# Kernel optimization log

Hardware: AMD Instinct MI355X
Metric: run time of the kernel (lower is better)

Reference implementation:

```python
import jax, jax.numpy as jnp
import numpy as np
from jax import lax

H = W = 96
C = 3
N_PIX = H * W
N_PER_CLASS = 50   # min(size_sample_fg=100 -> shuffled to min_samples, size_sample_bg=50)
K = 5
THRESHOLD = 0.3
POS_WEIGHT = 100.0
CLEAN_THRESH = 0.6


def _sample_idx(key, valid_mask_flat, n):
    # Uniform random sample of n indices from valid positions (fixed-shape
    # replacement for tf.random.shuffle(tf.where(mask))[:n]).
    u = jax.random.uniform(key, (N_PIX,))
    score = jnp.where(valid_mask_flat, u, -1.0)
    _, idx = lax.top_k(score, n)
    return idx


def _pixel_features(img01):
    # img01: [H, W, C] in [0, 1]. Matches: reshape(img)/255 concat weighted positions.
    img_flat = img01.reshape(-1, C) / 255.0
    ii, jj = jnp.meshgrid(jnp.arange(H), jnp.arange(W), indexing='ij')
    pos = jnp.stack([ii, jj], axis=-1).reshape(-1, 2).astype(jnp.float32)
    pos = pos / jnp.array([H, W], jnp.float32) * POS_WEIGHT
    return jnp.concatenate([img_flat, pos], axis=1)  # [N_PIX, C+2]


def _process_image(img, key):
    # preprocess: (already 96x96x3) normalize & clip
    img_p = jnp.clip(img / 255.0, 0.0, 1.0)

    # extract_image_tf: clean image, pick fg/bg scribble pixels
    img_norm = img_p / jnp.max(img_p, axis=(0, 1), keepdims=True)
    cleaned = img_norm * (img_norm < CLEAN_THRESH).astype(jnp.float32)
    fg = jnp.any(cleaned > 0, axis=-1).reshape(-1)  # [N_PIX] bool
    bg = ~fg
    k_fg, k_bg = jax.random.split(key)
    fg_idx = _sample_idx(k_fg, fg, N_PER_CLASS)
    bg_idx = _sample_idx(k_bg, bg, N_PER_CLASS)

    # extract_features_tf
    feats_all = _pixel_features(img_p)                       # [N_PIX, 5]
    train_feats = jnp.concatenate([feats_all[fg_idx], feats_all[bg_idx]], axis=0)  # [100, 5]
    train_labels = jnp.concatenate([jnp.ones(N_PER_CLASS), jnp.zeros(N_PER_CLASS)])

    # segment_image_KNN_tf: standardize, brute-force cdist, top-k, label vote
    mean = jnp.mean(train_feats, axis=0)
    std = jnp.std(train_feats, axis=0)
    train_s = (train_feats - mean) / std                     # [100, 5]
    test_s = (feats_all - mean) / std                        # [N_PIX, 5]
    dist = jnp.sqrt(jnp.sum(jnp.square(test_s[:, None, :] - train_s[None, :, :]), axis=2))  # [N_PIX, 100]
    _, knn_idx = lax.top_k(-dist, K)                         # smallest-k distances
    probas = jnp.mean(train_labels[knn_idx], axis=1)         # [N_PIX]
    seg = (probas >= THRESHOLD).astype(jnp.int32).reshape(H, W)

    # mask original (preprocessed) image
    return jnp.where(seg[..., None] == 1, img_p, jnp.zeros_like(img_p))


def setup_inputs() -> dict:
    key = jax.random.key(0)
    images = jax.random.uniform(key, (32, H, W, C), dtype=jnp.float32)
    return {"images": images}


def reference(images):
    B = images.shape[0]
    keys = jax.random.split(jax.random.key(42), B)
    return jax.vmap(_process_image)(images, keys)
```

## Files before the change

### kernel.cpp

```cpp
#include <hip/hip_runtime.h>
#include <stdint.h>

#define NPIX 9216
#define NIMG 32

__device__ __forceinline__ uint32_t rotl32(uint32_t x, int d){ return (x<<d)|(x>>(32-d)); }

__device__ __forceinline__ void threefry(uint32_t k0, uint32_t k1, uint32_t x0, uint32_t x1,
                                         uint32_t &o0, uint32_t &o1){
  uint32_t ks2 = k0 ^ k1 ^ 0x1BD11BDAu;
  x0 += k0; x1 += k1;
  x0+=x1; x1=rotl32(x1,13); x1^=x0;
  x0+=x1; x1=rotl32(x1,15); x1^=x0;
  x0+=x1; x1=rotl32(x1,26); x1^=x0;
  x0+=x1; x1=rotl32(x1,6);  x1^=x0;
  x0+=k1; x1+=ks2+1u;
  x0+=x1; x1=rotl32(x1,17); x1^=x0;
  x0+=x1; x1=rotl32(x1,29); x1^=x0;
  x0+=x1; x1=rotl32(x1,16); x1^=x0;
  x0+=x1; x1=rotl32(x1,24); x1^=x0;
  x0+=ks2; x1+=k0+2u;
  x0+=x1; x1=rotl32(x1,13); x1^=x0;
  x0+=x1; x1=rotl32(x1,15); x1^=x0;
  x0+=x1; x1=rotl32(x1,26); x1^=x0;
  x0+=x1; x1=rotl32(x1,6);  x1^=x0;
  x0+=k0; x1+=k1+3u;
  x0+=x1; x1=rotl32(x1,17); x1^=x0;
  x0+=x1; x1=rotl32(x1,29); x1^=x0;
  x0+=x1; x1=rotl32(x1,16); x1^=x0;
  x0+=x1; x1=rotl32(x1,24); x1^=x0;
  x0+=k1; x1+=ks2+4u;
  x0+=x1; x1=rotl32(x1,13); x1^=x0;
  x0+=x1; x1=rotl32(x1,15); x1^=x0;
  x0+=x1; x1=rotl32(x1,26); x1^=x0;
  x0+=x1; x1=rotl32(x1,6);  x1^=x0;
  x0+=ks2; x1+=k0+5u;
  o0=x0; o1=x1;
}

__device__ __forceinline__ float clip01_div255(float x){
  return fminf(fmaxf(x/255.0f, 0.0f), 1.0f);
}

__global__ __launch_bounds__(1024) void kprep(const float* __restrict__ in,
                                              float* __restrict__ ts2g,
                                              float* __restrict__ meanstd){
#pragma clang fp contract(off)
  int img = blockIdx.x;
  int tid = threadIdx.x;

  __shared__ uint32_t vvL[NPIX];
  __shared__ uint64_t cand[2048];
  __shared__ int      hist[2][129];
  __shared__ int      nc, bbinL[2];
  __shared__ float    cmaxL[3];
  __shared__ float    wred[3][16];
  __shared__ int      tIdx[100];
  __shared__ float    feat[100][5];
  __shared__ float    mv[5], sv[5];

  if(tid<258) ((int*)hist)[tid]=0;

  const float* p = in + (size_t)img*NPIX*3;

  {
    float m0=0.f, m1=0.f, m2=0.f;
    for(int k=0;k<9;k++){
      int px = k*1024 + tid;
      m0 = fmaxf(m0, clip01_div255(p[px*3+0]));
      m1 = fmaxf(m1, clip01_div255(p[px*3+1]));
      m2 = fmaxf(m2, clip01_div255(p[px*3+2]));
    }
    for(int off=32; off>0; off>>=1){
      m0 = fmaxf(m0, __shfl_down(m0,off));
      m1 = fmaxf(m1, __shfl_down(m1,off));
      m2 = fmaxf(m2, __shfl_down(m2,off));
    }
    int lane = tid & 63, wv = tid >> 6;
    if(lane==0){ wred[0][wv]=m0; wred[1][wv]=m1; wred[2][wv]=m2; }
  }
  __syncthreads();
  if(tid<3){
    float m = wred[tid][0];
    for(int w=1;w<16;w++) m = fmaxf(m, wred[tid][w]);
    cmaxL[tid]=m;
  }
  __syncthreads();
  float c0=cmaxL[0], c1=cmaxL[1], c2=cmaxL[2];

  uint32_t ik0, ik1; threefry(0u, 42u, 0u, (uint32_t)img, ik0, ik1);
  uint32_t sf0, sf1; threefry(ik0, ik1, 0u, 0u, sf0, sf1);
  uint32_t sb0, sb1; threefry(ik0, ik1, 0u, 1u, sb0, sb1);

  for(int k=0;k<9;k++){
    int px = k*1024 + tid;
    float a  = clip01_div255(p[px*3+0])/c0;
    float bb = clip01_div255(p[px*3+1])/c1;
    float c  = clip01_div255(p[px*3+2])/c2;
    bool fg = (a>0.f && a<0.6f) || (bb>0.f && bb<0.6f) || (c>0.f && c<0.6f);
    uint32_t k0 = fg ? sf0 : sb0, k1 = fg ? sf1 : sb1;
    uint32_t r1, r2; threefry(k0, k1, 0u, (uint32_t)px, r1, r2);
    uint32_t vv = ((r1 ^ r2) >> 9) + 1u;
    vvL[px] = vv | (fg ? 0x80000000u : 0u);
    atomicAdd(&hist[fg?0:1][vv>>16], 1);
  }
  __syncthreads();

  if(tid<128){
    int cls = tid>>6, l = tid&63;
    int h0 = hist[cls][2*l];
    int h1 = hist[cls][2*l+1];
    int h128 = hist[cls][128];
    int S = h0 + h1;
    for(int off=1; off<64; off<<=1){
      int o = __shfl_down(S, off);
      if(l + off < 64) S += o;
    }
    int ss0 = S + h128;
    int ss1 = S - h0 + h128;
    int cd = -1;
    if(ss0 >= 50) cd = 2*l;
    if(ss1 >= 50) cd = 2*l+1;
    if(l==63 && h128 >= 50) cd = 128;
    for(int off=32; off>0; off>>=1){
      int o = __shfl_down(cd, off);
      cd = o > cd ? o : cd;
    }
    if(l==0) bbinL[cls] = cd;
  }
  __syncthreads();

  for(int cls=0; cls<2; cls++){
    if(tid==0) nc=0;
    __syncthreads();
    int bb = bbinL[cls];
    uint32_t want = (cls==0) ? 0x80000000u : 0u;
    for(int k=0;k<9;k++){
      int px = k*1024 + tid;
      uint32_t w = vvL[px];
      if((w & 0x80000000u) == want){
        uint32_t vv = w & 0x7FFFFFFFu;
        if((int)(vv>>16) >= bb){
          int pos = atomicAdd(&nc,1);
          if(pos < 2048)
            cand[pos] = ((uint64_t)vv << 14) | (uint64_t)(16383 - px);
        }
      }
    }
    __syncthreads();
    int m = nc; if(m > 2048) m = 2048;
    for(int c=tid; c<m; c+=1024){
      uint64_t kk = cand[c];
      int r = 0, j = 0;
      while(j < m){
        int je = j+64 < m ? j+64 : m;
        for(; j<je; j++) r += (cand[j] > kk);
        if(r >= 50) break;
      }
      if(r < 50) tIdx[cls*50 + r] = 16383 - (int)(kk & 16383u);
    }
    __syncthreads();
    if(bb == -1){
      if(tid==0){
        int need = 50 - m, r = m;
        for(int px=0; px<NPIX && need>0; px++){
          if((vvL[px] & 0x80000000u) != want){ tIdx[cls*50 + r] = px; r++; need--; }
        }
      }
      __syncthreads();
    }
  }

  if(tid<100){
    int pp = tIdx[tid];
    int i=pp/96, j=pp-i*96;
    const float* px = in + ((size_t)img*NPIX + pp)*3;
    for(int c=0;c<3;c++){
      float ip=clip01_div255(px[c]);
      feat[tid][c]=ip/255.0f;
    }
    feat[tid][3]=((float)i/96.0f)*100.0f;
    feat[tid][4]=((float)j/96.0f)*100.0f;
  }
  __syncthreads();
  if(tid<5){
    float s=0.f;
    for(int r=0;r<100;r++) s=s+feat[r][tid];
    float mu=s/100.0f; mv[tid]=mu;
    float v=0.f;
    for(int r=0;r<100;r++){ float d=feat[r][tid]-mu; float q=d*d; v=v+q; }
    sv[tid]=sqrtf(v/100.0f);
  }
  __syncthreads();
  if(tid<100){
    float r0=(feat[tid][0]-mv[0])/sv[0];
    float r1=(feat[tid][1]-mv[1])/sv[1];
    float r2=(feat[tid][2]-mv[2])/sv[2];
    float r3=(feat[tid][3]-mv[3])/sv[3];
    float r4=(feat[tid][4]-mv[4])/sv[4];
    float* dst = ts2g + img*600 + (tid>>1)*12 + (tid&1);
    dst[0]=r0; dst[2]=r1; dst[4]=r2; dst[6]=r3; dst[8]=r4;
  }
  if(tid<5)       meanstd[img*10+tid]=mv[tid];
  else if(tid<10) meanstd[img*10+tid]=sv[tid-5];
}

__global__ __launch_bounds__(256) void kknn(const float* __restrict__ in,
                                            const float* __restrict__ ts2g,
                                            const float* __restrict__ meanstd,
                                            float* __restrict__ out){
#pragma clang fp contract(off)
  int b     = blockIdx.x;
  int img   = b / 36;
  int chunk = b % 36;
  int tid   = threadIdx.x;

  __shared__ float    mv[5], sv[5];
  __shared__ __attribute__((aligned(16))) float ts2[600];
  __shared__ __attribute__((aligned(16))) float pix[768];

  if(tid<150) ((float4*)ts2)[tid] = ((const float4*)(ts2g + img*600))[tid];
  if(tid>=192 && tid<197) mv[tid-192]=meanstd[img*10+(tid-192)];
  if(tid>=224 && tid<229) sv[tid-224]=meanstd[img*10+5+(tid-224)];
  {
    const float4* cb4 = (const float4*)(in + ((size_t)img*NPIX + (size_t)chunk*256)*3);
    if(tid<192) ((float4*)pix)[tid] = cb4[tid];
  }
  __syncthreads();

  int p = chunk*256+tid;
  int i=p/96, j=p-i*96;
  float ip0=clip01_div255(pix[tid*3+0]);
  float ip1=clip01_div255(pix[tid*3+1]);
  float ip2=clip01_div255(pix[tid*3+2]);
  float t0,t1,t2,t3,t4;
  {
    float f0=ip0/255.0f, f1=ip1/255.0f, f2=ip2/255.0f;
    float f3=((float)i/96.0f)*100.0f, f4=((float)j/96.0f)*100.0f;
    t0=(f0-mv[0])/sv[0]; t1=(f1-mv[1])/sv[1]; t2=(f2-mv[2])/sv[2];
    t3=(f3-mv[3])/sv[3]; t4=(f4-mv[4])/sv[4];
  }

  float a0x=1e30f,a0y=1e30f, a1x=1e30f,a1y=1e30f;
#pragma unroll 5
  for(int pr=0;pr<25;pr++){
    const float* tp = &ts2[pr*12];
    float4 qA = *(const float4*)(tp);
    float4 qB = *(const float4*)(tp+4);
    float2 qC = *(const float2*)(tp+8);
    float sx, sy;
    { float dx=t0-qA.x, dy=t0-qA.y; sx=dx*dx; sy=dy*dy; }
    { float dx=t1-qA.z, dy=t1-qA.w; float wx=dx*dx, wy=dy*dy; sx=sx+wx; sy=sy+wy; }
    { float dx=t2-qB.x, dy=t2-qB.y; float wx=dx*dx, wy=dy*dy; sx=sx+wx; sy=sy+wy; }
    { float dx=t3-qB.z, dy=t3-qB.w; float wx=dx*dx, wy=dy*dy; sx=sx+wx; sy=sy+wy; }
    { float dx=t4-qC.x, dy=t4-qC.y; float wx=dx*dx, wy=dy*dy; sx=sx+wx; sy=sy+wy; }
    float tx=fmaxf(a0x,sx), ty=fmaxf(a0y,sy);
    a0x=fminf(a0x,sx);      a0y=fminf(a0y,sy);
    a1x=fminf(a1x,tx);      a1y=fminf(a1y,ty);
  }
  float a1 = fmaxf(fminf(a0x,a1y), fminf(a1x,a0y));

  float b0x=1e30f,b0y=1e30f, b1x=1e30f,b1y=1e30f;
  float b2x=1e30f,b2y=1e30f, b3x=1e30f,b3y=1e30f;
#pragma unroll 5
  for(int pr=25;pr<50;pr++){
    const float* tp = &ts2[pr*12];
    float4 qA = *(const float4*)(tp);
    float4 qB = *(const float4*)(tp+4);
    float2 qC = *(const float2*)(tp+8);
    float sx, sy;
    { float dx=t0-qA.x, dy=t0-qA.y; sx=dx*dx; sy=dy*dy; }
    { float dx=t1-qA.z, dy=t1-qA.w; float wx=dx*dx, wy=dy*dy; sx=sx+wx; sy=sy+wy; }
    { float dx=t2-qB.x, dy=t2-qB.y; float wx=dx*dx, wy=dy*dy; sx=sx+wx; sy=sy+wy; }
    { float dx=t3-qB.z, dy=t3-qB.w; float wx=dx*dx, wy=dy*dy; sx=sx+wx; sy=sy+wy; }
    { float dx=t4-qC.x, dy=t4-qC.y; float wx=dx*dx, wy=dy*dy; sx=sx+wx; sy=sy+wy; }
    float u0x=fmaxf(b0x,sx), u0y=fmaxf(b0y,sy);
    b0x=fminf(b0x,sx);       b0y=fminf(b0y,sy);
    float u1x=fmaxf(b1x,u0x), u1y=fmaxf(b1y,u0y);
    b1x=fminf(b1x,u0x);       b1y=fminf(b1y,u0y);
    float u2x=fmaxf(b2x,u1x), u2y=fmaxf(b2y,u1y);
    b2x=fminf(b2x,u1x);       b2y=fminf(b2y,u1y);
    b3x=fminf(b3x,u2x);       b3y=fminf(b3y,u2y);
  }
  float l0=fminf(b0x,b3y), l1=fminf(b1x,b2y), l2=fminf(b2x,b1y), l3=fminf(b3x,b0y);
  float b3 = fmaxf(fmaxf(l0,l1), fmaxf(l2,l3));

  bool seg = sqrtf(a1) <= sqrtf(b3);
  __syncthreads();
  pix[tid*3+0]=seg?ip0:0.f;
  pix[tid*3+1]=seg?ip1:0.f;
  pix[tid*3+2]=seg?ip2:0.f;
  __syncthreads();
  float4* ob4 = (float4*)(out + ((size_t)img*NPIX + (size_t)chunk*256)*3);
  if(tid<192) ob4[tid] = ((float4*)pix)[tid];
}

extern "C" void kernel_launch(void* const* d_in, const int* in_sizes, int n_in,
                              void* d_out, int out_size, void* d_ws, size_t ws_size,
                              hipStream_t stream) {
  const float* in = (const float*)d_in[0];
  float* out = (float*)d_out;
  float* ts2g    = (float*)d_ws;
  float* meanstd = (float*)((char*)d_ws + 76800);

  kprep<<<32,   1024, 0, stream>>>(in, ts2g, meanstd);
  kknn <<<1152, 256,  0, stream>>>(in, ts2g, meanstd, out);
}
```

Before: 117.6 us.

## Vectorize image loads into registers and merge fg/bg candidate selection passes

The image is now read once with float4 loads and kept in registers, so the per-pixel scoring pass no longer issues a second set of strided scalar global loads. The two per-class candidate-collection passes are merged into a single sweep with separate counters and buffers. The rank-selection step then runs for both classes at once on two halves of the block, which removes several barriers. In exchange, each class's candidate buffer shrinks from 2048 to 1024 entries, so large candidate sets are truncated sooner, and register pressure rises.

```diff
diff --git a/kernel.cpp b/kernel.cpp
--- a/kernel.cpp
+++ b/kernel.cpp
@@ -50,9 +50,10 @@
   int tid = threadIdx.x;
 
   __shared__ uint32_t vvL[NPIX];
-  __shared__ uint64_t cand[2048];
+  __shared__ uint64_t cand[2][1024];
+  __shared__ int      ncA[2];
   __shared__ int      hist[2][129];
-  __shared__ int      nc, bbinL[2];
+  __shared__ int      bbinL[2];
   __shared__ float    cmaxL[3];
   __shared__ float    wred[3][16];
   __shared__ int      tIdx[100];
@@ -60,25 +61,34 @@
   __shared__ float    mv[5], sv[5];
 
   if(tid<258) ((int*)hist)[tid]=0;
+  if(tid<2)   ncA[tid]=0;
 
   const float* p = in + (size_t)img*NPIX*3;
-
-  {
-    float m0=0.f, m1=0.f, m2=0.f;
-    for(int k=0;k<9;k++){
-      int px = k*1024 + tid;
-      m0 = fmaxf(m0, clip01_div255(p[px*3+0]));
-      m1 = fmaxf(m1, clip01_div255(p[px*3+1]));
-      m2 = fmaxf(m2, clip01_div255(p[px*3+2]));
-    }
-    for(int off=32; off>0; off>>=1){
-      m0 = fmaxf(m0, __shfl_down(m0,off));
-      m1 = fmaxf(m1, __shfl_down(m1,off));
-      m2 = fmaxf(m2, __shfl_down(m2,off));
-    }
-    int lane = tid & 63, wv = tid >> 6;
-    if(lane==0){ wred[0][wv]=m0; wred[1][wv]=m1; wred[2][wv]=m2; }
-  }
+  const float4* ip4 = (const float4*)p;
+
+  float4 rv[3][3];
+  float m0=0.f, m1=0.f, m2=0.f;
+#pragma unroll
+  for(int k=0;k<3;k++){
+    int g = k*1024 + tid;
+    if(g < 2304){
+      float4 v0 = ip4[3*g+0], v1 = ip4[3*g+1], v2 = ip4[3*g+2];
+      rv[k][0]=v0; rv[k][1]=v1; rv[k][2]=v2;
+      m0 = fmaxf(m0, fmaxf(fmaxf(clip01_div255(v0.x), clip01_div255(v0.w)),
+                           fmaxf(clip01_div255(v1.z), clip01_div255(v2.y))));
+      m1 = fmaxf(m1, fmaxf(fmaxf(clip01_div255(v0.y), clip01_div255(v1.x)),
+                           fmaxf(clip01_div255(v1.w), clip01_div255(v2.z))));
+      m2 = fmaxf(m2, fmaxf(fmaxf(clip01_div255(v0.z), clip01_div255(v1.y)),
+                           fmaxf(clip01_div255(v2.x), clip01_div255(v2.w))));
+    }
+  }
+  for(int off=32; off>0; off>>=1){
+    m0 = fmaxf(m0, __shfl_down(m0,off));
+    m1 = fmaxf(m1, __shfl_down(m1,off));
+    m2 = fmaxf(m2, __shfl_down(m2,off));
+  }
+  { int lane = tid & 63, wv = tid >> 6;
+    if(lane==0){ wred[0][wv]=m0; wred[1][wv]=m1; wred[2][wv]=m2; } }
   __syncthreads();
   if(tid<3){
     float m = wred[tid][0];
@@ -92,17 +102,28 @@
   uint32_t sf0, sf1; threefry(ik0, ik1, 0u, 0u, sf0, sf1);
   uint32_t sb0, sb1; threefry(ik0, ik1, 0u, 1u, sb0, sb1);
 
-  for(int k=0;k<9;k++){
-    int px = k*1024 + tid;
-    float a  = clip01_div255(p[px*3+0])/c0;
-    float bb = clip01_div255(p[px*3+1])/c1;
-    float c  = clip01_div255(p[px*3+2])/c2;
+  auto score_px = [&](int px, float pa, float pb, float pc){
+    float a  = clip01_div255(pa)/c0;
+    float bb = clip01_div255(pb)/c1;
+    float c  = clip01_div255(pc)/c2;
     bool fg = (a>0.f && a<0.6f) || (bb>0.f && bb<0.6f) || (c>0.f && c<0.6f);
     uint32_t k0 = fg ? sf0 : sb0, k1 = fg ? sf1 : sb1;
     uint32_t r1, r2; threefry(k0, k1, 0u, (uint32_t)px, r1, r2);
     uint32_t vv = ((r1 ^ r2) >> 9) + 1u;
     vvL[px] = vv | (fg ? 0x80000000u : 0u);
     atomicAdd(&hist[fg?0:1][vv>>16], 1);
+  };
+#pragma unroll
+  for(int k=0;k<3;k++){
+    int g = k*1024 + tid;
+    if(g < 2304){
+      float4 v0=rv[k][0], v1=rv[k][1], v2=rv[k][2];
+      int pb = g*4;
+      score_px(pb+0, v0.x, v0.y, v0.z);
+      score_px(pb+1, v0.w, v1.x, v1.y);
+      score_px(pb+2, v1.z, v1.w, v2.x);
+      score_px(pb+3, v2.y, v2.z, v2.w);
+    }
   }
   __syncthreads();
 
@@ -130,38 +151,46 @@
   }
   __syncthreads();
 
-  for(int cls=0; cls<2; cls++){
-    if(tid==0) nc=0;
-    __syncthreads();
-    int bb = bbinL[cls];
-    uint32_t want = (cls==0) ? 0x80000000u : 0u;
+  {
+    int bb0 = bbinL[0], bb1 = bbinL[1];
     for(int k=0;k<9;k++){
       int px = k*1024 + tid;
       uint32_t w = vvL[px];
-      if((w & 0x80000000u) == want){
-        uint32_t vv = w & 0x7FFFFFFFu;
-        if((int)(vv>>16) >= bb){
-          int pos = atomicAdd(&nc,1);
-          if(pos < 2048)
-            cand[pos] = ((uint64_t)vv << 14) | (uint64_t)(16383 - px);
-        }
+      int cls = (w & 0x80000000u) ? 0 : 1;
+      uint32_t vv = w & 0x7FFFFFFFu;
+      int bb = cls ? bb1 : bb0;
+      if((int)(vv>>16) >= bb){
+        int pos = atomicAdd(&ncA[cls],1);
+        if(pos < 1024)
+          cand[cls][pos] = ((uint64_t)vv << 14) | (uint64_t)(16383 - px);
       }
     }
-    __syncthreads();
-    int m = nc; if(m > 2048) m = 2048;
-    for(int c=tid; c<m; c+=1024){
-      uint64_t kk = cand[c];
+  }
+  __syncthreads();
+
+  {
+    int cls = (tid >= 512);
+    int lt  = tid & 511;
+    int m = ncA[cls]; if(m > 1024) m = 1024;
+    const uint64_t* C = cand[cls];
+    for(int c=lt; c<m; c+=512){
+      uint64_t kk = C[c];
       int r = 0, j = 0;
       while(j < m){
         int je = j+64 < m ? j+64 : m;
-        for(; j<je; j++) r += (cand[j] > kk);
+        for(; j<je; j++) r += (C[j] > kk);
         if(r >= 50) break;
       }
       if(r < 50) tIdx[cls*50 + r] = 16383 - (int)(kk & 16383u);
     }
-    __syncthreads();
-    if(bb == -1){
+  }
+  __syncthreads();
+
+  for(int cls=0; cls<2; cls++){
+    if(bbinL[cls] == -1){
+      uint32_t want = (cls==0) ? 0x80000000u : 0u;
       if(tid==0){
+        int m = ncA[cls];
         int need = 50 - m, r = m;
         for(int px=0; px<NPIX && need>0; px++){
           if((vvL[px] & 0x80000000u) != want){ tIdx[cls*50 + r] = px; r++; need--; }
```

Measured after the change: 108.4 us. 7.9% less time.
